# Kernel optimization log

Measured on AMD Instinct MI355X. Metric: run time of the kernel, lower is better.

Reference implementation:

```python
import jax, jax.numpy as jnp
import numpy as np
import math

B, T, D, H = 4, 2048, 1024, 16
HD = D // H  # 64

def setup_inputs() -> dict:
    key = jax.random.key(0)
    ks = jax.random.split(key, 11)
    s = 1.0 / math.sqrt(D)
    return {
        "q": jax.random.normal(ks[0], (B, T, D), jnp.float32),
        "k": jax.random.normal(ks[1], (B, T, D), jnp.float32),
        "v": jax.random.normal(ks[2], (B, T, D), jnp.float32),
        "Wq": jax.random.normal(ks[3], (D, D), jnp.float32) * s,
        "bq": jnp.zeros((D,), jnp.float32),
        "Wk": jax.random.normal(ks[4], (D, D), jnp.float32) * s,
        "bk": jnp.zeros((D,), jnp.float32),
        "Wv": jax.random.normal(ks[5], (D, D), jnp.float32) * s,
        "bv": jnp.zeros((D,), jnp.float32),
        "Wo": jax.random.normal(ks[6], (D, D), jnp.float32) * s,
        "bo": jnp.zeros((D,), jnp.float32),
    }

def reference(q, k, v, Wq, bq, Wk, bk, Wv, bv, Wo, bo):
    # Linear projections (torch Linear: x @ W.T + b)
    qp = q @ Wq.T + bq
    kp = k @ Wk.T + bk
    vp = v @ Wv.T + bv
    # [B, T, D] -> [B, H, T, HD]
    def split(x):
        return x.reshape(B, T, H, HD).transpose(0, 2, 1, 3)
    qh, kh, vh = split(qp), split(kp), split(vp)
    # scaled dot-product attention
    score = jnp.einsum('bhqd,bhkd->bhqk', qh, kh) / math.sqrt(HD)
    attn = jax.nn.softmax(score, axis=-1)
    out = jnp.einsum('bhqk,bhkd->bhqd', attn, vh)
    # merge heads and output projection
    out = out.transpose(0, 2, 1, 3).reshape(B, T, D)
    return out @ Wo.T + bo
```

## Files before the change

kernel.cpp:

```cpp
#include <hip/hip_runtime.h>
#include <hip/hip_bf16.h>
#include <stdint.h>

#define B_ 4
#define T_ 2048
#define D_ 1024
#define H_ 16
#define HD_ 64
#define NKT (T_ / 64)

typedef __bf16 bf16;
typedef __bf16 bf16x8 __attribute__((ext_vector_type(8)));
typedef __bf16 bf16x4 __attribute__((ext_vector_type(4)));
typedef float f32x4 __attribute__((ext_vector_type(4)));
typedef uint32_t u32x4 __attribute__((ext_vector_type(4)));

#define QSCALE 0.18033688011112042f

__device__ __forceinline__ float fast_exp2(float x) {
#if __has_builtin(__builtin_amdgcn_exp2f)
    return __builtin_amdgcn_exp2f(x);
#else
    return exp2f(x);
#endif
}

__device__ __forceinline__ void async_load16(const bf16* g, const bf16* lds_uniform) {
    __builtin_amdgcn_global_load_lds(
        (const __attribute__((address_space(1))) uint32_t*)(uintptr_t)g,
        (__attribute__((address_space(3))) uint32_t*)(uintptr_t)lds_uniform,
        16, 0, 0);
}

__device__ __forceinline__ uint32_t pack2_bf16(float lo, float hi) {
    union { uint32_t u; __bf16 h[2]; } r;
    r.h[0] = (__bf16)lo;
    r.h[1] = (__bf16)hi;
    return r.u;
}

__device__ __forceinline__ void permswap16(uint32_t& a, uint32_t& b) {
    asm("v_permlane16_swap_b32 %0, %1" : "+v"(a), "+v"(b));
}

__global__ __launch_bounds__(256) void cast3(const float* __restrict__ s0, bf16* __restrict__ d0,
                                             const float* __restrict__ s1, bf16* __restrict__ d1,
                                             const float* __restrict__ s2, bf16* __restrict__ d2,
                                             int n4) {
    const float* s = blockIdx.y == 0 ? s0 : (blockIdx.y == 1 ? s1 : s2);
    bf16* d = blockIdx.y == 0 ? d0 : (blockIdx.y == 1 ? d1 : d2);
    int i = blockIdx.x * 256 + threadIdx.x;
    if (i < n4) {
        f32x4 v = ((const f32x4*)s)[i];
        bf16x4 o;
        o.x = (bf16)v.x; o.y = (bf16)v.y; o.z = (bf16)v.z; o.w = (bf16)v.w;
        ((bf16x4*)d)[i] = o;
    }
}

__global__ __launch_bounds__(256) void cast4(const float* __restrict__ s0, bf16* __restrict__ d0,
                                             const float* __restrict__ s1, bf16* __restrict__ d1,
                                             const float* __restrict__ s2, bf16* __restrict__ d2,
                                             const float* __restrict__ s3, bf16* __restrict__ d3,
                                             int n4) {
    const float* s = blockIdx.y == 0 ? s0 : (blockIdx.y == 1 ? s1 : (blockIdx.y == 2 ? s2 : s3));
    bf16* d = blockIdx.y == 0 ? d0 : (blockIdx.y == 1 ? d1 : (blockIdx.y == 2 ? d2 : d3));
    int i = blockIdx.x * 256 + threadIdx.x;
    if (i < n4) {
        f32x4 v = ((const f32x4*)s)[i];
        bf16x4 o;
        o.x = (bf16)v.x; o.y = (bf16)v.y; o.z = (bf16)v.z; o.w = (bf16)v.w;
        ((bf16x4*)d)[i] = o;
    }
}

template <typename OutT, int VMODE>
__device__ __forceinline__ void gemm_body(const bf16* __restrict__ A,
                                          const bf16* __restrict__ W,
                                          const float* __restrict__ bias,
                                          OutT* __restrict__ C,
                                          int lin, float scale,
                                          bf16* As, bf16* Bs, bf16* Tt) {
    const int K = D_, N = D_;
    const int tid = threadIdx.x;
    const int wid = tid >> 6, lane = tid & 63;
    const int quad = lane >> 4, l15 = lane & 15;
    const int wm = (wid >> 1) * 64, wn = (wid & 1) * 64;
    const int bx = N >> 7;
    const int ty = (lin & 7) + 8 * (lin / (8 * bx));
    const int tx = (lin >> 3) % bx;
    const long rowA0 = (long)ty * 128;
    const long rowB0 = (long)tx * 128;
    const int srow = lane >> 2;
    const int schunk = (lane & 3) * 8;
    const int sbase = (wid * 32) * 32;

    f32x4 acc[4][4];
#pragma unroll
    for (int i = 0; i < 4; i++)
#pragma unroll
        for (int j = 0; j < 4; j++) acc[i][j] = (f32x4){0.f, 0.f, 0.f, 0.f};

#pragma unroll
    for (int s = 0; s < 2; s++) {
        int r = wid * 32 + s * 16 + srow;
        async_load16(&A[(rowA0 + r) * K + schunk], &As[sbase + s * 16 * 32]);
        async_load16(&W[(rowB0 + r) * K + schunk], &Bs[sbase + s * 16 * 32]);
    }
    __syncthreads();

    const int NIT = K >> 5;
    for (int it = 0; it < NIT; it++) {
        const int cur = it & 1;
        const int co = cur * (128 * 32);
        if (it + 1 < NIT) {
            const int k1 = (it + 1) << 5;
            const int no = (cur ^ 1) * (128 * 32);
#pragma unroll
            for (int s = 0; s < 2; s++) {
                int r = wid * 32 + s * 16 + srow;
                async_load16(&A[(rowA0 + r) * K + k1 + schunk], &As[no + sbase + s * 16 * 32]);
                async_load16(&W[(rowB0 + r) * K + k1 + schunk], &Bs[no + sbase + s * 16 * 32]);
            }
        }
        bf16x8 af[4], bfr[4];
#pragma unroll
        for (int i = 0; i < 4; i++)
            af[i] = *(const bf16x8*)&As[co + (wm + i * 16 + l15) * 32 + quad * 8];
#pragma unroll
        for (int j = 0; j < 4; j++)
            bfr[j] = *(const bf16x8*)&Bs[co + (wn + j * 16 + l15) * 32 + quad * 8];
#pragma unroll
        for (int i = 0; i < 4; i++)
#pragma unroll
            for (int j = 0; j < 4; j++)
                acc[i][j] = __builtin_amdgcn_mfma_f32_16x16x32_bf16(af[i], bfr[j],
                                                                    acc[i][j], 0, 0, 0);
        __syncthreads();
    }

    if constexpr (VMODE == 0) {
#pragma unroll
        for (int i = 0; i < 4; i++) {
            long m = rowA0 + wm + i * 16 + quad * 4;
#pragma unroll
            for (int j = 0; j < 4; j++) {
                long n = rowB0 + wn + j * 16 + l15;
                float bb = bias[n];
#pragma unroll
                for (int r = 0; r < 4; r++) {
                    float v = (acc[i][j][r] + bb) * scale;
                    C[(m + r) * N + n] = (OutT)v;
                }
            }
        }
    } else {
#pragma unroll
        for (int i = 0; i < 4; i++) {
            int ml = wm + i * 16 + quad * 4;
#pragma unroll
            for (int j = 0; j < 4; j++) {
                int nl = wn + j * 16 + l15;
                float bb = bias[rowB0 + nl];
                bf16x4 ov = {(bf16)(acc[i][j][0] + bb), (bf16)(acc[i][j][1] + bb),
                             (bf16)(acc[i][j][2] + bb), (bf16)(acc[i][j][3] + bb)};
                *(bf16x4*)&Tt[nl * 136 + ml] = ov;
            }
        }
        __syncthreads();
        const long bidx = rowA0 >> 11;
        const int t0 = (int)(rowA0 & 2047);
#pragma unroll
        for (int p = 0; p < 8; p++) {
            int nl = p * 16 + (tid >> 4);
            int c = tid & 15;
            bf16x8 val = *(const bf16x8*)&Tt[nl * 136 + c * 8];
            int n = (int)rowB0 + nl;
            long vrow = (bidx * H_ + (n >> 6)) * (long)HD_ + (n & 63);
            int cp = (c & ~3) | ((c & 1) << 1) | ((c & 2) >> 1);
            *(bf16x8*)&((bf16*)C)[vrow * T_ + t0 + cp * 8] = val;
        }
    }
}

__global__ __launch_bounds__(256) void gemm_qkv(const bf16* __restrict__ Xq,
                                                const bf16* __restrict__ WqB,
                                                const float* __restrict__ bq,
                                                bf16* __restrict__ Qp,
                                                const bf16* __restrict__ Xk,
                                                const bf16* __restrict__ WkB,
                                                const float* __restrict__ bk,
                                                bf16* __restrict__ Kp,
                                                const bf16* __restrict__ Xv,
                                                const bf16* __restrict__ WvB,
                                                const float* __restrict__ bv,
                                                bf16* __restrict__ VtG) {
    __shared__ __align__(16) char sm[34816];
    bf16* As = (bf16*)sm;
    bf16* Bs = (bf16*)(sm + 16384);
    bf16* Tt = (bf16*)sm;
    const int p = blockIdx.x >> 9;
    const int lin = blockIdx.x & 511;
    if (p == 0)
        gemm_body<bf16, 0>(Xq, WqB, bq, Qp, lin, QSCALE, As, Bs, Tt);
    else if (p == 1)
        gemm_body<bf16, 0>(Xk, WkB, bk, Kp, lin, 1.f, As, Bs, Tt);
    else
        gemm_body<bf16, 1>(Xv, WvB, bv, VtG, lin, 1.f, As, Bs, Tt);
}

__global__ __launch_bounds__(256) void gemm_out(const bf16* __restrict__ Op,
                                                const bf16* __restrict__ WoB,
                                                const float* __restrict__ bo,
                                                float* __restrict__ out) {
    __shared__ __align__(16) char sm[32768];
    bf16* As = (bf16*)sm;
    bf16* Bs = (bf16*)(sm + 16384);
    gemm_body<float, 0>(Op, WoB, bo, out, blockIdx.x, 1.f, As, Bs, nullptr);
}

__global__ __launch_bounds__(512, 8) void attn_kernel(const bf16* __restrict__ Qp,
                                                      const bf16* __restrict__ Kp,
                                                      const bf16* __restrict__ VT,
                                                      bf16* __restrict__ Op) {
    __shared__ bf16 smem[4][64 * 64];
    const int tid = threadIdx.x;
    const int wid = tid >> 6, lane = tid & 63;
    const int quad = lane >> 4, l15 = lane & 15;
    const int q7 = l15 & 7;
    const int lin = blockIdx.x;
    const int bh = (lin & 7) + 8 * (lin >> 7);
    const int qt = (lin >> 3) & 15;
    const int b = bh >> 4, h = bh & 15;
    const long tok0 = (long)b * T_ + (long)qt * 128 + wid * 16;
    const int hcol = h * HD_;
    const long vrow0 = ((long)bh) * HD_;
    const int g_sw = ((lane & 7) ^ (lane >> 3)) * 8;
    const int srow = lane >> 3;
    const int sbase = (wid * 8) * 64;

    {
        const long krow0 = (long)b * T_;
        const int r = wid * 8 + srow;
        async_load16(&Kp[(krow0 + r) * D_ + hcol + g_sw], &smem[0][sbase]);
        async_load16(&VT[(vrow0 + r) * T_ + g_sw], &smem[2][sbase]);
    }

    bf16x8 bq0 = *(const bf16x8*)&Qp[(tok0 + l15) * D_ + hcol + quad * 8];
    bf16x8 bq1 = *(const bf16x8*)&Qp[(tok0 + l15) * D_ + hcol + 32 + quad * 8];

    const u32x4 onesu = {0x3F803F80u, 0x3F803F80u, 0x3F803F80u, 0x3F803F80u};
    const bf16x8 ones = __builtin_bit_cast(bf16x8, onesu);

    f32x4 o[4];
#pragma unroll
    for (int mt = 0; mt < 4; mt++) o[mt] = (f32x4){0.f, 0.f, 0.f, 0.f};
    f32x4 ls = (f32x4){0.f, 0.f, 0.f, 0.f};

    __syncthreads();

    for (int kt = 0; kt < NKT; kt++) {
        const int cur = kt & 1;
        if (kt + 1 < NKT) {
            const long krow1 = (long)b * T_ + (long)(kt + 1) * 64;
            const int nb = cur ^ 1;
            const int r = wid * 8 + srow;
            async_load16(&Kp[(krow1 + r) * D_ + hcol + g_sw], &smem[nb][sbase]);
            async_load16(&VT[(vrow0 + r) * T_ + (long)(kt + 1) * 64 + g_sw],
                         &smem[2 + nb][sbase]);
        }
        const bf16* Ksc = smem[cur];
        const bf16* Vsc = smem[2 + cur];

        bf16x8 pb0;
        {
            uint32_t pA[2], pB[2];
#pragma unroll
            for (int mt = 0; mt < 2; mt++) {
                bf16x8 ak0 = *(const bf16x8*)&Ksc[(mt * 16 + l15) * 64 + ((quad ^ q7) * 8)];
                bf16x8 ak1 = *(const bf16x8*)&Ksc[(mt * 16 + l15) * 64 + (((4 + quad) ^ q7) * 8)];
                f32x4 s = {0.f, 0.f, 0.f, 0.f};
                s = __builtin_amdgcn_mfma_f32_16x16x32_bf16(ak0, bq0, s, 0, 0, 0);
                s = __builtin_amdgcn_mfma_f32_16x16x32_bf16(ak1, bq1, s, 0, 0, 0);
                float p0 = fast_exp2(s[0]), p1 = fast_exp2(s[1]);
                float p2 = fast_exp2(s[2]), p3 = fast_exp2(s[3]);
                pA[mt] = pack2_bf16(p0, p1);
                pB[mt] = pack2_bf16(p2, p3);
            }
            permswap16(pA[0], pA[1]);
            permswap16(pB[0], pB[1]);
            u32x4 f = {pA[0], pB[0], pA[1], pB[1]};
            pb0 = __builtin_bit_cast(bf16x8, f);
        }
        __builtin_amdgcn_s_setprio(1);
        ls = __builtin_amdgcn_mfma_f32_16x16x32_bf16(ones, pb0, ls, 0, 0, 0);
#pragma unroll
        for (int mt = 0; mt < 4; mt++) {
            bf16x8 av0 = *(const bf16x8*)&Vsc[(mt * 16 + l15) * 64 + ((quad ^ q7) * 8)];
            o[mt] = __builtin_amdgcn_mfma_f32_16x16x32_bf16(av0, pb0, o[mt], 0, 0, 0);
        }
        __builtin_amdgcn_s_setprio(0);
        bf16x8 pb1;
        {
            uint32_t pA[2], pB[2];
#pragma unroll
            for (int mt = 0; mt < 2; mt++) {
                bf16x8 ak0 = *(const bf16x8*)&Ksc[((2 + mt) * 16 + l15) * 64 + ((quad ^ q7) * 8)];
                bf16x8 ak1 = *(const bf16x8*)&Ksc[((2 + mt) * 16 + l15) * 64 +
                                                  (((4 + quad) ^ q7) * 8)];
                f32x4 s = {0.f, 0.f, 0.f, 0.f};
                s = __builtin_amdgcn_mfma_f32_16x16x32_bf16(ak0, bq0, s, 0, 0, 0);
                s = __builtin_amdgcn_mfma_f32_16x16x32_bf16(ak1, bq1, s, 0, 0, 0);
                float p0 = fast_exp2(s[0]), p1 = fast_exp2(s[1]);
                float p2 = fast_exp2(s[2]), p3 = fast_exp2(s[3]);
                pA[mt] = pack2_bf16(p0, p1);
                pB[mt] = pack2_bf16(p2, p3);
            }
            permswap16(pA[0], pA[1]);
            permswap16(pB[0], pB[1]);
            u32x4 f = {pA[0], pB[0], pA[1], pB[1]};
            pb1 = __builtin_bit_cast(bf16x8, f);
        }
        __builtin_amdgcn_s_setprio(1);
        ls = __builtin_amdgcn_mfma_f32_16x16x32_bf16(ones, pb1, ls, 0, 0, 0);
#pragma unroll
        for (int mt = 0; mt < 4; mt++) {
            bf16x8 av1 = *(const bf16x8*)&Vsc[(mt * 16 + l15) * 64 + (((4 + quad) ^ q7) * 8)];
            o[mt] = __builtin_amdgcn_mfma_f32_16x16x32_bf16(av1, pb1, o[mt], 0, 0, 0);
        }
        __builtin_amdgcn_s_setprio(0);
        __syncthreads();
    }

    const float linv = 1.f / ls[0];

    bf16* ew = (bf16*)smem + wid * (16 * 64);
#pragma unroll
    for (int mt = 0; mt < 4; mt++) {
        bf16x4 ov = {(bf16)(o[mt][0] * linv), (bf16)(o[mt][1] * linv),
                     (bf16)(o[mt][2] * linv), (bf16)(o[mt][3] * linv)};
        *(bf16x4*)&ew[l15 * 64 + (((mt * 2 + (quad >> 1)) ^ q7) * 8) + (quad & 1) * 4] = ov;
    }
#pragma unroll
    for (int p2 = 0; p2 < 2; p2++) {
        int q = p2 * 8 + (lane >> 3);
        int dc = lane & 7;
        bf16x8 ov = *(const bf16x8*)&ew[q * 64 + ((dc ^ (q & 7)) * 8)];
        *(bf16x8*)&Op[(tok0 + q) * D_ + hcol + dc * 8] = ov;
    }
}

extern "C" void kernel_launch(void* const* d_in, const int* in_sizes, int n_in,
                              void* d_out, int out_size, void* d_ws, size_t ws_size,
                              hipStream_t stream) {
    const float* q  = (const float*)d_in[0];
    const float* k  = (const float*)d_in[1];
    const float* v  = (const float*)d_in[2];
    const float* Wq = (const float*)d_in[3];
    const float* bq = (const float*)d_in[4];
    const float* Wk = (const float*)d_in[5];
    const float* bk = (const float*)d_in[6];
    const float* Wv = (const float*)d_in[7];
    const float* bv = (const float*)d_in[8];
    const float* Wo = (const float*)d_in[9];
    const float* bo = (const float*)d_in[10];
    float* out = (float*)d_out;

    const size_t MD = (size_t)B_ * T_ * D_;
    const size_t DD = (size_t)D_ * D_;
    char* ws = (char*)d_ws;
    bf16* Xq  = (bf16*)ws; ws += MD * 2;
    bf16* Xk  = (bf16*)ws; ws += MD * 2;
    bf16* Xv  = (bf16*)ws; ws += MD * 2;
    bf16* WqB = (bf16*)ws; ws += DD * 2;
    bf16* WkB = (bf16*)ws; ws += DD * 2;
    bf16* WvB = (bf16*)ws; ws += DD * 2;
    bf16* WoB = (bf16*)ws; ws += DD * 2;
    bf16* Qp  = (bf16*)ws; ws += MD * 2;
    bf16* Kp  = (bf16*)ws; ws += MD * 2;
    bf16* VtG = (bf16*)ws; ws += MD * 2;
    bf16* Op  = (bf16*)ws; ws += MD * 2;

    cast3<<<dim3(MD / 4 / 256, 3), 256, 0, stream>>>(q, Xq, k, Xk, v, Xv, MD / 4);
    cast4<<<dim3(DD / 4 / 256, 4), 256, 0, stream>>>(Wq, WqB, Wk, WkB, Wv, WvB, Wo, WoB, DD / 4);

    gemm_qkv<<<3 * 512, 256, 0, stream>>>(Xq, WqB, bq, Qp, Xk, WkB, bk, Kp, Xv, WvB, bv, VtG);

    attn_kernel<<<B_ * H_ * (T_ / 128), 512, 0, stream>>>(Qp, Kp, VtG, Op);

    gemm_out<<<512, 256, 0, stream>>>(Op, WoB, bo, out);
}
```

Before: 339.1 us.

## Fuse activation fp32-to-bf16 cast into QKV GEMM loads and stagger attention halves

Removes the separate cast kernel for q/k/v. The QKV GEMM now loads fp32 activation tiles into registers, converts them to bf16 and writes them to LDS, overlapping the conversion with MFMA work. This avoids writing and re-reading bf16 copies of the inputs, but replaces the asynchronous global-to-LDS load for A with register staging, which adds VGPR pressure and doubles A bytes fetched per tile. The attention loop is also refactored into a lambda whose half order alternates by wave parity, spreading K/V LDS reads across waves.

Result: slower. 356.2 us (+5.0%).

```diff
diff --git a/kernel.cpp b/kernel.cpp
--- a/kernel.cpp
+++ b/kernel.cpp
@@ -14,6 +14,7 @@
 typedef __bf16 bf16x4 __attribute__((ext_vector_type(4)));
 typedef float f32x4 __attribute__((ext_vector_type(4)));
 typedef uint32_t u32x4 __attribute__((ext_vector_type(4)));
+typedef uint32_t u32x2 __attribute__((ext_vector_type(2)));
 
 #define QSCALE 0.18033688011112042f
 
@@ -41,21 +42,6 @@
 
 __device__ __forceinline__ void permswap16(uint32_t& a, uint32_t& b) {
     asm("v_permlane16_swap_b32 %0, %1" : "+v"(a), "+v"(b));
-}
-
-__global__ __launch_bounds__(256) void cast3(const float* __restrict__ s0, bf16* __restrict__ d0,
-                                             const float* __restrict__ s1, bf16* __restrict__ d1,
-                                             const float* __restrict__ s2, bf16* __restrict__ d2,
-                                             int n4) {
-    const float* s = blockIdx.y == 0 ? s0 : (blockIdx.y == 1 ? s1 : s2);
-    bf16* d = blockIdx.y == 0 ? d0 : (blockIdx.y == 1 ? d1 : d2);
-    int i = blockIdx.x * 256 + threadIdx.x;
-    if (i < n4) {
-        f32x4 v = ((const f32x4*)s)[i];
-        bf16x4 o;
-        o.x = (bf16)v.x; o.y = (bf16)v.y; o.z = (bf16)v.z; o.w = (bf16)v.w;
-        ((bf16x4*)d)[i] = o;
-    }
 }
 
 __global__ __launch_bounds__(256) void cast4(const float* __restrict__ s0, bf16* __restrict__ d0,
@@ -74,14 +60,16 @@
     }
 }
 
-template <typename OutT, int VMODE>
-__device__ __forceinline__ void gemm_body(const bf16* __restrict__ A,
+template <typename OutT, int VMODE, int AF32>
+__device__ __forceinline__ void gemm_body(const void* __restrict__ Av,
                                           const bf16* __restrict__ W,
                                           const float* __restrict__ bias,
                                           OutT* __restrict__ C,
                                           int lin, float scale,
                                           bf16* As, bf16* Bs, bf16* Tt) {
     const int K = D_, N = D_;
+    const bf16* Ab = (const bf16*)Av;
+    const float* Af = (const float*)Av;
     const int tid = threadIdx.x;
     const int wid = tid >> 6, lane = tid & 63;
     const int quad = lane >> 4, l15 = lane & 15;
@@ -93,6 +81,8 @@
     const long rowB0 = (long)tx * 128;
     const int srow = lane >> 2;
     const int schunk = (lane & 3) * 8;
+    const int srow4 = lane >> 3;
+    const int schunk4 = (lane & 7) * 4;
     const int sbase = (wid * 32) * 32;
 
     f32x4 acc[4][4];
@@ -101,11 +91,31 @@
 #pragma unroll
         for (int j = 0; j < 4; j++) acc[i][j] = (f32x4){0.f, 0.f, 0.f, 0.f};
 
-#pragma unroll
-    for (int s = 0; s < 2; s++) {
-        int r = wid * 32 + s * 16 + srow;
-        async_load16(&A[(rowA0 + r) * K + schunk], &As[sbase + s * 16 * 32]);
-        async_load16(&W[(rowB0 + r) * K + schunk], &Bs[sbase + s * 16 * 32]);
+    if constexpr (AF32) {
+        f32x4 a0[4];
+#pragma unroll
+        for (int s = 0; s < 4; s++) {
+            int r = wid * 32 + s * 8 + srow4;
+            a0[s] = *(const f32x4*)&Af[(rowA0 + r) * K + schunk4];
+        }
+#pragma unroll
+        for (int s = 0; s < 2; s++) {
+            int r = wid * 32 + s * 16 + srow;
+            async_load16(&W[(rowB0 + r) * K + schunk], &Bs[sbase + s * 16 * 32]);
+        }
+#pragma unroll
+        for (int s = 0; s < 4; s++) {
+            int r = wid * 32 + s * 8 + srow4;
+            u32x2 w2 = {pack2_bf16(a0[s].x, a0[s].y), pack2_bf16(a0[s].z, a0[s].w)};
+            *(u32x2*)&As[r * 32 + schunk4] = w2;
+        }
+    } else {
+#pragma unroll
+        for (int s = 0; s < 2; s++) {
+            int r = wid * 32 + s * 16 + srow;
+            async_load16(&Ab[(rowA0 + r) * K + schunk], &As[sbase + s * 16 * 32]);
+            async_load16(&W[(rowB0 + r) * K + schunk], &Bs[sbase + s * 16 * 32]);
+        }
     }
     __syncthreads();
 
@@ -113,14 +123,31 @@
     for (int it = 0; it < NIT; it++) {
         const int cur = it & 1;
         const int co = cur * (128 * 32);
+        const int no = (cur ^ 1) * (128 * 32);
+        f32x4 a_ld[4];
         if (it + 1 < NIT) {
             const int k1 = (it + 1) << 5;
-            const int no = (cur ^ 1) * (128 * 32);
-#pragma unroll
-            for (int s = 0; s < 2; s++) {
-                int r = wid * 32 + s * 16 + srow;
-                async_load16(&A[(rowA0 + r) * K + k1 + schunk], &As[no + sbase + s * 16 * 32]);
-                async_load16(&W[(rowB0 + r) * K + k1 + schunk], &Bs[no + sbase + s * 16 * 32]);
+            if constexpr (AF32) {
+#pragma unroll
+                for (int s = 0; s < 4; s++) {
+                    int r = wid * 32 + s * 8 + srow4;
+                    a_ld[s] = *(const f32x4*)&Af[(rowA0 + r) * K + k1 + schunk4];
+                }
+#pragma unroll
+                for (int s = 0; s < 2; s++) {
+                    int r = wid * 32 + s * 16 + srow;
+                    async_load16(&W[(rowB0 + r) * K + k1 + schunk],
+                                 &Bs[no + sbase + s * 16 * 32]);
+                }
+            } else {
+#pragma unroll
+                for (int s = 0; s < 2; s++) {
+                    int r = wid * 32 + s * 16 + srow;
+                    async_load16(&Ab[(rowA0 + r) * K + k1 + schunk],
+                                 &As[no + sbase + s * 16 * 32]);
+                    async_load16(&W[(rowB0 + r) * K + k1 + schunk],
+                                 &Bs[no + sbase + s * 16 * 32]);
+                }
             }
         }
         bf16x8 af[4], bfr[4];
@@ -136,6 +163,17 @@
             for (int j = 0; j < 4; j++)
                 acc[i][j] = __builtin_amdgcn_mfma_f32_16x16x32_bf16(af[i], bfr[j],
                                                                     acc[i][j], 0, 0, 0);
+        if constexpr (AF32) {
+            if (it + 1 < NIT) {
+#pragma unroll
+                for (int s = 0; s < 4; s++) {
+                    int r = wid * 32 + s * 8 + srow4;
+                    u32x2 w2 = {pack2_bf16(a_ld[s].x, a_ld[s].y),
+                                pack2_bf16(a_ld[s].z, a_ld[s].w)};
+                    *(u32x2*)&As[no + r * 32 + schunk4] = w2;
+                }
+            }
+        }
         __syncthreads();
     }
 
@@ -183,15 +221,15 @@
     }
 }
 
-__global__ __launch_bounds__(256) void gemm_qkv(const bf16* __restrict__ Xq,
+__global__ __launch_bounds__(256) void gemm_qkv(const float* __restrict__ q,
                                                 const bf16* __restrict__ WqB,
                                                 const float* __restrict__ bq,
                                                 bf16* __restrict__ Qp,
-                                                const bf16* __restrict__ Xk,
+                                                const float* __restrict__ k,
                                                 const bf16* __restrict__ WkB,
                                                 const float* __restrict__ bk,
                                                 bf16* __restrict__ Kp,
-                                                const bf16* __restrict__ Xv,
+                                                const float* __restrict__ v,
                                                 const bf16* __restrict__ WvB,
                                                 const float* __restrict__ bv,
                                                 bf16* __restrict__ VtG) {
@@ -202,11 +240,11 @@
     const int p = blockIdx.x >> 9;
     const int lin = blockIdx.x & 511;
     if (p == 0)
-        gemm_body<bf16, 0>(Xq, WqB, bq, Qp, lin, QSCALE, As, Bs, Tt);
+        gemm_body<bf16, 0, 1>(q, WqB, bq, Qp, lin, QSCALE, As, Bs, Tt);
     else if (p == 1)
-        gemm_body<bf16, 0>(Xk, WkB, bk, Kp, lin, 1.f, As, Bs, Tt);
+        gemm_body<bf16, 0, 1>(k, WkB, bk, Kp, lin, 1.f, As, Bs, Tt);
     else
-        gemm_body<bf16, 1>(Xv, WvB, bv, VtG, lin, 1.f, As, Bs, Tt);
+        gemm_body<bf16, 1, 1>(v, WvB, bv, VtG, lin, 1.f, As, Bs, Tt);
 }
 
 __global__ __launch_bounds__(256) void gemm_out(const bf16* __restrict__ Op,
@@ -216,7 +254,7 @@
     __shared__ __align__(16) char sm[32768];
     bf16* As = (bf16*)sm;
     bf16* Bs = (bf16*)(sm + 16384);
-    gemm_body<float, 0>(Op, WoB, bo, out, blockIdx.x, 1.f, As, Bs, nullptr);
+    gemm_body<float, 0, 0>(Op, WoB, bo, out, blockIdx.x, 1.f, As, Bs, nullptr);
 }
 
 __global__ __launch_bounds__(512, 8) void attn_kernel(const bf16* __restrict__ Qp,
@@ -259,6 +297,8 @@
 
     __syncthreads();
 
+    const int h0 = wid & 1;
+
     for (int kt = 0; kt < NKT; kt++) {
         const int cur = kt & 1;
         if (kt + 1 < NKT) {
@@ -272,13 +312,13 @@
         const bf16* Ksc = smem[cur];
         const bf16* Vsc = smem[2 + cur];
 
-        bf16x8 pb0;
-        {
+        auto half_step = [&](int hh) {
             uint32_t pA[2], pB[2];
 #pragma unroll
             for (int mt = 0; mt < 2; mt++) {
-                bf16x8 ak0 = *(const bf16x8*)&Ksc[(mt * 16 + l15) * 64 + ((quad ^ q7) * 8)];
-                bf16x8 ak1 = *(const bf16x8*)&Ksc[(mt * 16 + l15) * 64 + (((4 + quad) ^ q7) * 8)];
+                const bf16* kr = &Ksc[(hh * 32 + mt * 16 + l15) * 64];
+                bf16x8 ak0 = *(const bf16x8*)&kr[(quad ^ q7) * 8];
+                bf16x8 ak1 = *(const bf16x8*)&kr[((4 + quad) ^ q7) * 8];
                 f32x4 s = {0.f, 0.f, 0.f, 0.f};
                 s = __builtin_amdgcn_mfma_f32_16x16x32_bf16(ak0, bq0, s, 0, 0, 0);
                 s = __builtin_amdgcn_mfma_f32_16x16x32_bf16(ak1, bq1, s, 0, 0, 0);
@@ -290,45 +330,17 @@
             permswap16(pA[0], pA[1]);
             permswap16(pB[0], pB[1]);
             u32x4 f = {pA[0], pB[0], pA[1], pB[1]};
-            pb0 = __builtin_bit_cast(bf16x8, f);
-        }
-        __builtin_amdgcn_s_setprio(1);
-        ls = __builtin_amdgcn_mfma_f32_16x16x32_bf16(ones, pb0, ls, 0, 0, 0);
-#pragma unroll
-        for (int mt = 0; mt < 4; mt++) {
-            bf16x8 av0 = *(const bf16x8*)&Vsc[(mt * 16 + l15) * 64 + ((quad ^ q7) * 8)];
-            o[mt] = __builtin_amdgcn_mfma_f32_16x16x32_bf16(av0, pb0, o[mt], 0, 0, 0);
-        }
-        __builtin_amdgcn_s_setprio(0);
-        bf16x8 pb1;
-        {
-            uint32_t pA[2], pB[2];
-#pragma unroll
-            for (int mt = 0; mt < 2; mt++) {
-                bf16x8 ak0 = *(const bf16x8*)&Ksc[((2 + mt) * 16 + l15) * 64 + ((quad ^ q7) * 8)];
-                bf16x8 ak1 = *(const bf16x8*)&Ksc[((2 + mt) * 16 + l15) * 64 +
-                                                  (((4 + quad) ^ q7) * 8)];
-                f32x4 s = {0.f, 0.f, 0.f, 0.f};
-                s = __builtin_amdgcn_mfma_f32_16x16x32_bf16(ak0, bq0, s, 0, 0, 0);
-                s = __builtin_amdgcn_mfma_f32_16x16x32_bf16(ak1, bq1, s, 0, 0, 0);
-                float p0 = fast_exp2(s[0]), p1 = fast_exp2(s[1]);
-                float p2 = fast_exp2(s[2]), p3 = fast_exp2(s[3]);
-                pA[mt] = pack2_bf16(p0, p1);
-                pB[mt] = pack2_bf16(p2, p3);
-            }
-            permswap16(pA[0], pA[1]);
-            permswap16(pB[0], pB[1]);
-            u32x4 f = {pA[0], pB[0], pA[1], pB[1]};
-            pb1 = __builtin_bit_cast(bf16x8, f);
-        }
-        __builtin_amdgcn_s_setprio(1);
-        ls = __builtin_amdgcn_mfma_f32_16x16x32_bf16(ones, pb1, ls, 0, 0, 0);
-#pragma unroll
-        for (int mt = 0; mt < 4; mt++) {
-            bf16x8 av1 = *(const bf16x8*)&Vsc[(mt * 16 + l15) * 64 + (((4 + quad) ^ q7) * 8)];
-            o[mt] = __builtin_amdgcn_mfma_f32_16x16x32_bf16(av1, pb1, o[mt], 0, 0, 0);
-        }
-        __builtin_amdgcn_s_setprio(0);
+            bf16x8 pb = __builtin_bit_cast(bf16x8, f);
+            ls = __builtin_amdgcn_mfma_f32_16x16x32_bf16(ones, pb, ls, 0, 0, 0);
+            const int vch = ((hh * 4 + quad) ^ q7) * 8;
+#pragma unroll
+            for (int mt = 0; mt < 4; mt++) {
+                bf16x8 av = *(const bf16x8*)&Vsc[(mt * 16 + l15) * 64 + vch];
+                o[mt] = __builtin_amdgcn_mfma_f32_16x16x32_bf16(av, pb, o[mt], 0, 0, 0);
+            }
+        };
+        half_step(h0);
+        half_step(h0 ^ 1);
         __syncthreads();
     }
 
@@ -369,9 +381,6 @@
     const size_t MD = (size_t)B_ * T_ * D_;
     const size_t DD = (size_t)D_ * D_;
     char* ws = (char*)d_ws;
-    bf16* Xq  = (bf16*)ws; ws += MD * 2;
-    bf16* Xk  = (bf16*)ws; ws += MD * 2;
-    bf16* Xv  = (bf16*)ws; ws += MD * 2;
     bf16* WqB = (bf16*)ws; ws += DD * 2;
     bf16* WkB = (bf16*)ws; ws += DD * 2;
     bf16* WvB = (bf16*)ws; ws += DD * 2;
@@ -381,10 +390,9 @@
     bf16* VtG = (bf16*)ws; ws += MD * 2;
     bf16* Op  = (bf16*)ws; ws += MD * 2;
 
-    cast3<<<dim3(MD / 4 / 256, 3), 256, 0, stream>>>(q, Xq, k, Xk, v, Xv, MD / 4);
     cast4<<<dim3(DD / 4 / 256, 4), 256, 0, stream>>>(Wq, WqB, Wk, WkB, Wv, WvB, Wo, WoB, DD / 4);
 
-    gemm_qkv<<<3 * 512, 256, 0, stream>>>(Xq, WqB, bq, Qp, Xk, WkB, bk, Kp, Xv, WvB, bv, VtG);
+    gemm_qkv<<<3 * 512, 256, 0, stream>>>(q, WqB, bq, Qp, k, WkB, bk, Kp, v, WvB, bv, VtG);
 
     attn_kernel<<<B_ * H_ * (T_ / 128), 512, 0, stream>>>(Qp, Kp, VtG, Op);
 
```
